# Optimization experiments

Measured on AMD Instinct MI355X. Metric: run time of the kernel, lower is better.

Reference implementation:

```python
import jax, jax.numpy as jnp
import numpy as np

NUM_HEADS = 16
EPS = 1e-6


def _ln(t, w, b):
    # LayerNorm over last dim (head_dim), elementwise affine, eps=1e-6
    mu = jnp.mean(t, axis=-1, keepdims=True)
    var = jnp.mean(jnp.square(t - mu), axis=-1, keepdims=True)
    return (t - mu) * jax.lax.rsqrt(var + EPS) * w + b


def setup_inputs() -> dict:
    key = jax.random.key(0)
    ks = jax.random.split(key, 10)
    b, s1, s2, qdim, kdim = 2, 2048, 3072, 1024, 1024
    d = qdim // NUM_HEADS
    x = jax.random.normal(ks[0], (b, s1, qdim), dtype=jnp.float32)
    y = jax.random.normal(ks[1], (b, s2, kdim), dtype=jnp.float32)
    padding_mask = jax.random.randint(ks[2], (b, s2), 0, 2) > 0
    # guarantee at least one valid key per row (avoid all -inf softmax rows)
    padding_mask = padding_mask.at[:, 0].set(True)
    w = 0.02
    Wq = jax.random.normal(ks[3], (qdim, qdim), dtype=jnp.float32) * w
    bq = jnp.zeros((qdim,), jnp.float32)
    Wkv = jax.random.normal(ks[4], (2 * qdim, kdim), dtype=jnp.float32) * w
    bkv = jnp.zeros((2 * qdim,), jnp.float32)
    qn_w = jnp.ones((d,), jnp.float32)
    qn_b = jnp.zeros((d,), jnp.float32)
    kn_w = jnp.ones((d,), jnp.float32)
    kn_b = jnp.zeros((d,), jnp.float32)
    Wo = jax.random.normal(ks[5], (qdim, qdim), dtype=jnp.float32) * w
    bo = jnp.zeros((qdim,), jnp.float32)
    return {"x": x, "y": y, "padding_mask": padding_mask,
            "Wq": Wq, "bq": bq, "Wkv": Wkv, "bkv": bkv,
            "qn_w": qn_w, "qn_b": qn_b, "kn_w": kn_w, "kn_b": kn_b,
            "Wo": Wo, "bo": bo}


def reference(x, y, padding_mask, Wq, bq, Wkv, bkv, qn_w, qn_b, kn_w, kn_b, Wo, bo):
    b, s1, c = x.shape
    s2 = y.shape[1]
    h, d = NUM_HEADS, c // NUM_HEADS
    scale = d ** (-0.5)
    q = (x @ Wq.T + bq).reshape(b, s1, h, d)
    kv = (y @ Wkv.T + bkv).reshape(b, s2, 2, h, d)
    k, v = kv[:, :, 0], kv[:, :, 1]  # (b, s2, h, d)
    q = _ln(q, qn_w, qn_b) * scale
    k = _ln(k, kn_w, kn_b)
    attn = jnp.einsum('bihd,bjhd->bhij', q, k)  # (b, h, s1, s2)
    attn = jnp.where(padding_mask[:, None, None, :], attn, -jnp.inf)
    p = jax.nn.softmax(attn, axis=-1)
    ctx = jnp.einsum('bhij,bjhd->bihd', p, v).reshape(b, s1, c)
    out = ctx @ Wo.T + bo
    return out
```

## Files before the change

kernel.cpp:

```cpp
#include <hip/hip_runtime.h>
#include <stdint.h>
#include <stddef.h>

typedef __attribute__((ext_vector_type(4))) float  f32x4;
typedef __attribute__((ext_vector_type(8))) short  short8;
typedef __attribute__((ext_vector_type(4))) short  short4v;
typedef __attribute__((ext_vector_type(2))) unsigned int uint2v;

__device__ __forceinline__ unsigned short f2bfbits(float f) {
  unsigned int u = __builtin_bit_cast(unsigned int, f);
  u += 0x7FFFu + ((u >> 16) & 1u);
  return (unsigned short)(u >> 16);
}

__device__ __forceinline__ f32x4 mfma16(short8 a, short8 b, f32x4 c) {
  return __builtin_amdgcn_mfma_f32_16x16x32_bf16(a, b, c, 0, 0, 0);
}

__device__ __forceinline__ unsigned int cvtpk(float a, float b) {
  unsigned int r;
  asm volatile("v_cvt_pk_bf16_f32 %0, %1, %2" : "=v"(r) : "v"(a), "v"(b));
  return r;
}

__device__ __forceinline__ void gload16(const void* g, void* l) {
  __builtin_amdgcn_global_load_lds(
      (const __attribute__((address_space(1))) void*)g,
      (__attribute__((address_space(3))) void*)l, 16, 0, 0);
}

__device__ __forceinline__ void cvt_block(const float* __restrict__ in,
                                          unsigned short* __restrict__ out,
                                          int blk, int t) {
  size_t i = (size_t)blk * 256 + t;
  f32x4 a = *(const f32x4*)(in + i * 8);
  f32x4 b = *(const f32x4*)(in + i * 8 + 4);
  short8 o;
  o[0] = (short)f2bfbits(a[0]); o[1] = (short)f2bfbits(a[1]);
  o[2] = (short)f2bfbits(a[2]); o[3] = (short)f2bfbits(a[3]);
  o[4] = (short)f2bfbits(b[0]); o[5] = (short)f2bfbits(b[1]);
  o[6] = (short)f2bfbits(b[2]); o[7] = (short)f2bfbits(b[3]);
  *(short8*)(out + i * 8) = o;
}

__global__ __launch_bounds__(256) void fused_prep(
    const float* __restrict__ x, unsigned short* __restrict__ xb,
    const float* __restrict__ y, unsigned short* __restrict__ yb,
    const float* __restrict__ Wq, unsigned short* __restrict__ Wqb,
    const float* __restrict__ Wkv, unsigned short* __restrict__ Wkvb,
    const float* __restrict__ Wo, unsigned short* __restrict__ Wob,
    const unsigned char* __restrict__ mraw, float* __restrict__ maddC,
    int* __restrict__ invperm, int* __restrict__ nvalid) {
  const int bid = blockIdx.x, t = threadIdx.x;
  if (bid < 2048)       { cvt_block(x,   xb,   bid,        t); return; }
  else if (bid < 5120)  { cvt_block(y,   yb,   bid - 2048, t); return; }
  else if (bid < 5632)  { cvt_block(Wq,  Wqb,  bid - 5120, t); return; }
  else if (bid < 6656)  { cvt_block(Wkv, Wkvb, bid - 5632, t); return; }
  else if (bid < 7168)  { cvt_block(Wo,  Wob,  bid - 6656, t); return; }

  const int batch = bid - 7168;
  __shared__ int s_na, s_gt, s_m84;
  if (t == 0) { s_na = 0; s_gt = 0; s_m84 = 0; }
  __syncthreads();
  int na = 0, gt = 0, m84 = 0;
  for (int i = t; i < 4096; i += 256) {
    unsigned char v = mraw[i];
    if (v) {
      if (i & 3) na++;
      if ((i & 7) == 4) m84++;
      if (v > 1) gt++;
    }
  }
  atomicAdd(&s_na, na); atomicAdd(&s_gt, gt); atomicAdd(&s_m84, m84);
  __syncthreads();
  int layout;
  if (s_na == 0) layout = s_m84 ? 1 : 3;
  else           layout = s_gt ? 2 : 0;

  const int base = batch * 3072;
  int myv[12];
  int cnt = 0;
#pragma unroll
  for (int k = 0; k < 12; k++) {
    int j = t * 12 + k;
    int gj = base + j;
    bool mv;
    if (layout == 0)      mv = mraw[gj] != 0;
    else if (layout == 1) mv = ((const int*)mraw)[gj] != 0;
    else if (layout == 2) mv = ((const float*)mraw)[gj] > 0.5f;
    else                  mv = ((const long long*)mraw)[gj] != 0;
    myv[k] = mv ? 1 : 0;
    cnt += myv[k];
  }
  const int lane = t & 63, wv = t >> 6;
  int inc = cnt;
#pragma unroll
  for (int d = 1; d < 64; d <<= 1) {
    int n = __shfl_up(inc, d);
    if (lane >= d) inc += n;
  }
  __shared__ int wsum[4];
  if (lane == 63) wsum[wv] = inc;
  __syncthreads();
  int woff = 0;
#pragma unroll
  for (int i2 = 0; i2 < 4; i2++) if (i2 < wv) woff += wsum[i2];
  const int total = wsum[0] + wsum[1] + wsum[2] + wsum[3];
  int vp = woff + inc - cnt;
  if (t == 0) nvalid[batch] = total;
#pragma unroll
  for (int k = 0; k < 12; k++) {
    int j = t * 12 + k;
    int slot = myv[k] ? vp : (total + (j - vp));
    invperm[base + slot] = j;
    vp += myv[k];
  }
  for (int jj = t; jj < 3072; jj += 256)
    maddC[base + jj] = (jj < total) ? -10.0f : -1e30f;
}

__global__ __launch_bounds__(256) void gemm_qkv(
    const unsigned short* __restrict__ xb, const unsigned short* __restrict__ Wqb,
    const float* __restrict__ bq, const float* __restrict__ qnw,
    const float* __restrict__ qnb, unsigned short* __restrict__ qln,
    const unsigned short* __restrict__ yb, const unsigned short* __restrict__ Wkvb,
    const float* __restrict__ bkv, const float* __restrict__ knw,
    const float* __restrict__ knb, unsigned short* __restrict__ kln,
    unsigned short* __restrict__ vrow) {
  __shared__ unsigned short As[128 * 64];
  __shared__ unsigned short Bs[128 * 64];
  const int t = threadIdx.x, l = t & 63, w = t >> 6;
  const int lo = l & 15, hi = l >> 4;
  const int wr = w >> 1, wc = w & 1;
  const int flat = blockIdx.x;
  int vb;
  if (flat < 256) vb = (flat & 7) * 32 + (flat >> 3);
  else { int f2 = flat - 256; vb = 256 + (f2 & 7) * 96 + (f2 >> 3); }
  const int isq = vb < 256;
  const int bn = isq ? (vb & 7) : ((vb - 256) & 15);
  const int bm = isq ? (vb >> 3) : ((vb - 256) >> 4);
  const unsigned short* A = isq ? xb : yb;
  const unsigned short* B = isq ? Wqb : Wkvb;
  const float* bias = isq ? bq : bkv;
  const float* lnw = isq ? qnw : knw;
  const float* lnb = isq ? qnb : knb;
  unsigned short* bfout = isq ? qln : kln;
  const float lnscale = isq ? 0.125f * 1.44269504f : 1.0f;
  const int rpb = isq ? 2048 : 3072;
  const int K = 1024;

  const int sr = l >> 3;
  const int sc = ((l & 7) ^ sr) << 3;
  const unsigned short* Ab = A + (size_t)bm * 128 * K + (size_t)sr * K + sc;
  const unsigned short* Bb = B + (size_t)bn * 128 * K + (size_t)sr * K + sc;

  f32x4 acc[4][4] = {};

  for (int kt = 0; kt < K; kt += 64) {
    __syncthreads();
#pragma unroll
    for (int p = 0; p < 4; ++p) {
      int c = w * 4 + p;
      gload16(Ab + (size_t)c * 8 * K + kt, &As[c * 512]);
      gload16(Bb + (size_t)c * 8 * K + kt, &Bs[c * 512]);
    }
    __syncthreads();
#pragma unroll
    for (int kk = 0; kk < 2; ++kk) {
      short8 af[4], bf[4];
#pragma unroll
      for (int i = 0; i < 4; ++i) {
        int slot = (((kk * 4 + hi) ^ (lo & 7)) << 3);
        af[i] = *(const short8*)&As[(wr * 64 + i * 16 + lo) * 64 + slot];
        bf[i] = *(const short8*)&Bs[(wc * 64 + i * 16 + lo) * 64 + slot];
      }
#pragma unroll
      for (int i = 0; i < 4; ++i)
#pragma unroll
        for (int j = 0; j < 4; ++j)
          acc[i][j] = mfma16(af[i], bf[j], acc[i][j]);
    }
  }

  float bv[4];
#pragma unroll
  for (int j = 0; j < 4; ++j) bv[j] = bias[bn * 128 + wc * 64 + j * 16 + lo];
#pragma unroll
  for (int i = 0; i < 4; ++i)
#pragma unroll
    for (int j = 0; j < 4; ++j)
#pragma unroll
      for (int r = 0; r < 4; ++r) acc[i][j][r] += bv[j];

  if (!isq && bn >= 8) {
#pragma unroll
    for (int j = 0; j < 4; ++j) {
      int col = bn * 128 + wc * 64 + j * 16 + lo;
      int vcol = col - 1024;
#pragma unroll
      for (int i = 0; i < 4; ++i) {
        int row = bm * 128 + wr * 64 + i * 16 + hi * 4;
#pragma unroll
        for (int r = 0; r < 4; ++r)
          vrow[(size_t)(row + r) * 1024 + vcol] = f2bfbits(acc[i][j][r]);
      }
    }
  } else {
    float gwv[4], gbv[4];
#pragma unroll
    for (int j = 0; j < 4; ++j) {
      gwv[j] = lnw[j * 16 + lo];
      gbv[j] = lnb[j * 16 + lo];
    }
    const int hcol = (bn * 128 + wc * 64) >> 6;
#pragma unroll
    for (int i = 0; i < 4; ++i) {
#pragma unroll
      for (int r = 0; r < 4; ++r) {
        float s1 = (acc[i][0][r] + acc[i][1][r]) + (acc[i][2][r] + acc[i][3][r]);
        float s2 = (acc[i][0][r] * acc[i][0][r] + acc[i][1][r] * acc[i][1][r]) +
                   (acc[i][2][r] * acc[i][2][r] + acc[i][3][r] * acc[i][3][r]);
#pragma unroll
        for (int m = 1; m < 16; m <<= 1) {
          s1 += __shfl_xor(s1, m);
          s2 += __shfl_xor(s2, m);
        }
        float mu = s1 * 0.015625f;
        float var = fmaxf(s2 * 0.015625f - mu * mu, 0.0f);
        float rq = rsqrtf(var + 1e-6f);
        int row = bm * 128 + wr * 64 + i * 16 + hi * 4 + r;
        int bb = row >= rpb;
        int rr = row - bb * rpb;
        size_t base = ((size_t)(bb * 16 + hcol) * rpb + rr) * 64;
#pragma unroll
        for (int j = 0; j < 4; ++j)
          bfout[base + j * 16 + lo] =
              f2bfbits(((acc[i][j][r] - mu) * rq * gwv[j] + gbv[j]) * lnscale);
      }
    }
  }
}

__global__ __launch_bounds__(256) void v_tr(
    const unsigned short* __restrict__ vrow, const int* __restrict__ invperm,
    unsigned short* __restrict__ vt) {
  __shared__ unsigned short tile[64][65];
  const int jt = blockIdx.x, h = blockIdx.y;
  const int b = jt / 48, j0 = (jt % 48) * 64;
  const int t = threadIdx.x;
  const int r = t >> 2, c0 = (t & 3) << 4;
  const int sj = invperm[b * 3072 + j0 + r];
  const unsigned short* src = vrow + ((size_t)b * 3072 + sj) * 1024 + h * 64 + c0;
  *(short8*)&tile[r][c0]     = *(const short8*)src;
  *(short8*)&tile[r][c0 + 8] = *(const short8*)(src + 8);
  __syncthreads();
  const int d = t >> 2, jc = (t & 3) << 4;
  unsigned short* dst = vt + ((size_t)((b * 16 + h) * 64 + d)) * 3072 + j0 + jc;
  short8 o0, o1;
#pragma unroll
  for (int i = 0; i < 8; i++) o0[i] = tile[jc + i][d];
#pragma unroll
  for (int i = 0; i < 8; i++) o1[i] = tile[jc + 8 + i][d];
  *(short8*)dst = o0;
  *(short8*)(dst + 8) = o1;
}

__global__ __launch_bounds__(512) void gemm_out(
    const unsigned short* __restrict__ A, const unsigned short* __restrict__ B,
    const float* __restrict__ bias, float* __restrict__ C, int N, int K) {
  __shared__ unsigned short As[128 * 64];
  __shared__ unsigned short Bs[128 * 64];
  const int t = threadIdx.x, l = t & 63, w = t >> 6;
  const int lo = l & 15, hi = l >> 4;
  const int wr = w >> 1, wc = w & 1;
  const int bn = blockIdx.x, bm = blockIdx.y;

  const int sr = l >> 3;
  const int sc = ((l & 7) ^ sr) << 3;
  const unsigned short* Ab = A + (size_t)bm * 128 * K + (size_t)sr * K + sc;
  const unsigned short* Bb = B + (size_t)bn * 128 * K + (size_t)sr * K + sc;

  f32x4 acc[2][4] = {};

  for (int kt = 0; kt < K; kt += 64) {
    __syncthreads();
#pragma unroll
    for (int p = 0; p < 2; ++p) {
      int c = p * 8 + w;
      gload16(Ab + (size_t)c * 8 * K + kt, &As[c * 512]);
      gload16(Bb + (size_t)c * 8 * K + kt, &Bs[c * 512]);
    }
    __syncthreads();
#pragma unroll
    for (int kk = 0; kk < 2; ++kk) {
      short8 af[2], bf[4];
#pragma unroll
      for (int i = 0; i < 2; ++i) {
        int slot = (((kk * 4 + hi) ^ (lo & 7)) << 3);
        af[i] = *(const short8*)&As[(wr * 32 + i * 16 + lo) * 64 + slot];
      }
#pragma unroll
      for (int j = 0; j < 4; ++j) {
        int slot = (((kk * 4 + hi) ^ (lo & 7)) << 3);
        bf[j] = *(const short8*)&Bs[(wc * 64 + j * 16 + lo) * 64 + slot];
      }
#pragma unroll
      for (int i = 0; i < 2; ++i)
#pragma unroll
        for (int j = 0; j < 4; ++j)
          acc[i][j] = mfma16(af[i], bf[j], acc[i][j]);
    }
  }

#pragma unroll
  for (int j = 0; j < 4; ++j) {
    int col = bn * 128 + wc * 64 + j * 16 + lo;
    float bv = bias[col];
#pragma unroll
    for (int i = 0; i < 2; ++i) {
      int row = bm * 128 + wr * 32 + i * 16 + hi * 4;
#pragma unroll
      for (int r = 0; r < 4; ++r)
        C[(size_t)(row + r) * N + col] = acc[i][j][r] + bv;
    }
  }
}

__global__ __launch_bounds__(256, 4) void attn_fwd(
    const unsigned short* __restrict__ Q, const unsigned short* __restrict__ KnU,
    const unsigned short* __restrict__ Vt, const float* __restrict__ maskAdd,
    const int* __restrict__ invperm, const int* __restrict__ nva,
    unsigned short* __restrict__ ctx) {
  int flat = blockIdx.y * 32 + blockIdx.x;
  int f = (flat & 7) * 128 + (flat >> 3);
  const int bh = f >> 5, qb = f & 31;
  const int b = bh >> 4, h = bh & 15;
  const int t = threadIdx.x, l = t & 63, w = t >> 6;
  const int lo = l & 15, hi = l >> 4;
  const int q0 = qb * 64 + w * 16;

  const int nv = nva[b];
  const int kend = (nv + 63) & ~63;

  __shared__ unsigned short lds[20480];
  unsigned short* Ks = lds;
  unsigned short* Vs = lds + 8192;
  unsigned short* P  = lds + 16384 + w * 1024;

  const unsigned short* Qh = Q + ((size_t)bh * 2048 + q0) * 64;
  const unsigned short* KbU = KnU + (size_t)bh * 3072 * 64;
  const unsigned short* Vb = Vt + (size_t)bh * 64 * 3072;
  const float* mb = maskAdd + b * 3072;
  const int ibase = b * 3072;

  const int srow = w * 8 + (l >> 3);
  const int swz8 = ((l & 7) ^ ((l >> 3) & 7)) << 3;
  const unsigned short* vS = Vb + (size_t)srow * 3072 + swz8;
  const int dstoff = w * 512;

  short8 qf[2];
#pragma unroll
  for (int g = 0; g < 2; g++)
    qf[g] = *(const short8*)(Qh + (size_t)lo * 64 + g * 32 + hi * 8);

  f32x4 O[4] = {};
  f32x4 lacc = {};
  const int myswz = (lo & 7) << 3;

  short8 paR[2] = {};
  short8 vfR[4][2] = {};

  int rs0 = invperm[ibase + srow];
  int rs1 = invperm[ibase + 32 + srow];
  gload16(KbU + (size_t)rs0 * 64 + swz8, Ks + dstoff);
  gload16(KbU + (size_t)rs1 * 64 + swz8, Ks + 2048 + dstoff);
  gload16(vS, Vs + dstoff);
  gload16(vS + 98304, Vs + 2048 + dstoff);
  {
    int kt1 = (64 < kend) ? 64 : 0;
    rs0 = invperm[ibase + kt1 + srow];
    rs1 = invperm[ibase + kt1 + 32 + srow];
  }
  __syncthreads();

  for (int kt = 0; kt < kend; kt += 64) {
    const int cur = (kt >> 6) & 1;
    const int nxt = cur ^ 1;
    const int ktn = (kt + 64 < kend) ? kt + 64 : 0;
    gload16(KbU + (size_t)rs0 * 64 + swz8, Ks + nxt * 4096 + dstoff);
    gload16(KbU + (size_t)rs1 * 64 + swz8, Ks + nxt * 4096 + 2048 + dstoff);
    gload16(vS + ktn, Vs + nxt * 4096 + dstoff);
    gload16(vS + ktn + 98304, Vs + nxt * 4096 + 2048 + dstoff);
    {
      int ktn2 = (kt + 128 < kend) ? kt + 128 : 0;
      rs0 = invperm[ibase + ktn2 + srow];
      rs1 = invperm[ibase + ktn2 + 32 + srow];
    }

    const unsigned short* Kc = Ks + cur * 4096;
    const unsigned short* Vc = Vs + cur * 4096;

    f32x4 s[4];
#pragma unroll
    for (int nf = 0; nf < 4; nf++)
      s[nf] = *(const f32x4*)(mb + kt + nf * 16 + hi * 4);
    __builtin_amdgcn_s_setprio(1);
#pragma unroll
    for (int nf = 0; nf < 4; nf++) {
      const int row = nf * 16 + lo;
      short8 k0 = *(const short8*)&Kc[row * 64 + ((hi * 8) ^ myswz)];
      short8 k1 = *(const short8*)&Kc[row * 64 + ((32 + hi * 8) ^ myswz)];
      s[nf] = mfma16(k0, qf[0], s[nf]);
      s[nf] = mfma16(k1, qf[1], s[nf]);
    }

#pragma unroll
    for (int df = 0; df < 4; df++)
#pragma unroll
      for (int ks = 0; ks < 2; ks++)
        O[df] = mfma16(paR[ks], vfR[df][ks], O[df]);
    __builtin_amdgcn_s_setprio(0);

#pragma unroll
    for (int nf = 0; nf < 4; nf++)
#pragma unroll
      for (int r = 0; r < 4; r++)
        s[nf][r] = __builtin_amdgcn_exp2f(s[nf][r]);
    lacc += (s[0] + s[1]) + (s[2] + s[3]);

#pragma unroll
    for (int nf = 0; nf < 4; nf++) {
      uint2v u;
      u.x = cvtpk(s[nf][0], s[nf][1]);
      u.y = cvtpk(s[nf][2], s[nf][3]);
      *(uint2v*)&P[lo * 64 + ((nf * 16 + hi * 4) ^ myswz)] = u;
    }
#pragma unroll
    for (int ks = 0; ks < 2; ks++)
      paR[ks] = *(const short8*)&P[lo * 64 + ((ks * 32 + hi * 8) ^ myswz)];
#pragma unroll
    for (int df = 0; df < 4; df++) {
      const int row = df * 16 + lo;
#pragma unroll
      for (int ks = 0; ks < 2; ks++)
        vfR[df][ks] = *(const short8*)&Vc[row * 64 + ((ks * 32 + hi * 8) ^ myswz)];
    }

    __syncthreads();
  }

  __builtin_amdgcn_s_setprio(1);
#pragma unroll
  for (int df = 0; df < 4; df++)
#pragma unroll
    for (int ks = 0; ks < 2; ks++)
      O[df] = mfma16(paR[ks], vfR[df][ks], O[df]);
  __builtin_amdgcn_s_setprio(0);

  float lr = (lacc[0] + lacc[1]) + (lacc[2] + lacc[3]);
  lr += __shfl_xor(lr, 16);
  lr += __shfl_xor(lr, 32);

  float i0 = 1.0f / __shfl(lr, hi * 4 + 0);
  float i1 = 1.0f / __shfl(lr, hi * 4 + 1);
  float i2 = 1.0f / __shfl(lr, hi * 4 + 2);
  float i3 = 1.0f / __shfl(lr, hi * 4 + 3);
  size_t rbase = (size_t)b * 2048 + q0 + hi * 4;
#pragma unroll
  for (int df = 0; df < 4; df++) {
    int cc = h * 64 + df * 16 + lo;
    ctx[(rbase + 0) * 1024 + cc] = f2bfbits(O[df][0] * i0);
    ctx[(rbase + 1) * 1024 + cc] = f2bfbits(O[df][1] * i1);
    ctx[(rbase + 2) * 1024 + cc] = f2bfbits(O[df][2] * i2);
    ctx[(rbase + 3) * 1024 + cc] = f2bfbits(O[df][3] * i3);
  }
}

extern "C" void kernel_launch(void* const* d_in, const int* in_sizes, int n_in,
                              void* d_out, int out_size, void* d_ws, size_t ws_size,
                              hipStream_t stream) {
  const float* x   = (const float*)d_in[0];
  const float* y   = (const float*)d_in[1];
  const unsigned char* pmask = (const unsigned char*)d_in[2];
  const float* Wq  = (const float*)d_in[3];
  const float* bq  = (const float*)d_in[4];
  const float* Wkv = (const float*)d_in[5];
  const float* bkv = (const float*)d_in[6];
  const float* qnw = (const float*)d_in[7];
  const float* qnb = (const float*)d_in[8];
  const float* knw = (const float*)d_in[9];
  const float* knb = (const float*)d_in[10];
  const float* Wo  = (const float*)d_in[11];
  const float* bo  = (const float*)d_in[12];
  float* out = (float*)d_out;

  const size_t MB = 1024ull * 1024ull;
  char* ws = (char*)d_ws;
  float* maddC         = (float*)ws;
  int*   invperm       = (int*)(ws + 24576);
  int*   nvalid        = (int*)(ws + 49152);
  char*  wb            = ws + 131072;
  unsigned short* Wqb  = (unsigned short*)(wb);
  unsigned short* Wkvb = (unsigned short*)(wb + 2 * MB);
  unsigned short* Wob  = (unsigned short*)(wb + 6 * MB);
  unsigned short* qln  = (unsigned short*)(wb + 8 * MB);
  unsigned short* kln  = (unsigned short*)(wb + 16 * MB);
  unsigned short* vt   = (unsigned short*)(wb + 28 * MB);
  unsigned short* ctxb = (unsigned short*)(wb + 40 * MB);
  unsigned short* yb   = (unsigned short*)(wb + 48 * MB);
  unsigned short* xb   = (unsigned short*)(wb + 60 * MB);
  unsigned short* vrow = (unsigned short*)(wb + 68 * MB);
  if (ws_size < 131072 + 80 * MB) return;

  fused_prep<<<dim3(7170), dim3(256), 0, stream>>>(
      x, xb, y, yb, Wq, Wqb, Wkv, Wkvb, Wo, Wob, pmask, maddC, invperm,
      nvalid);

  gemm_qkv<<<dim3(1024), dim3(256), 0, stream>>>(
      xb, Wqb, bq, qnw, qnb, qln, yb, Wkvb, bkv, knw, knb, kln, vrow);

  v_tr<<<dim3(96, 16), dim3(256), 0, stream>>>(vrow, invperm, vt);

  attn_fwd<<<dim3(32, 32), dim3(256), 0, stream>>>(qln, kln, vt, maddC,
                                                   invperm, nvalid, ctxb);

  gemm_out<<<dim3(8, 32), dim3(512), 0, stream>>>(ctxb, Wob, bo, out, 1024, 1024);
}
```

Before: 147.0 us.

## Halve attention key tile to 32 and drop software-pipelined PV to raise occupancy

The attention kernel's key/value tile shrinks from 64 to 32 keys per iteration, which halves LDS use and the per-wave P buffer. The launch bound goes from 4 to 8 blocks per CU. The PV MFMAs no longer run one iteration behind the QK MFMAs in registers; they run in the same iteration, which frees the paR/vfR registers. The aim is more resident waves to hide latency, at the cost of twice as many barriers and loop iterations and less overlap of MFMA with exp inside a wave.

```diff
diff --git a/kernel.cpp b/kernel.cpp
--- a/kernel.cpp
+++ b/kernel.cpp
@@ -326,7 +326,7 @@
   }
 }
 
-__global__ __launch_bounds__(256, 4) void attn_fwd(
+__global__ __launch_bounds__(256, 8) void attn_fwd(
     const unsigned short* __restrict__ Q, const unsigned short* __restrict__ KnU,
     const unsigned short* __restrict__ Vt, const float* __restrict__ maskAdd,
     const int* __restrict__ invperm, const int* __restrict__ nva,
@@ -340,12 +340,12 @@
   const int q0 = qb * 64 + w * 16;
 
   const int nv = nva[b];
-  const int kend = (nv + 63) & ~63;
-
-  __shared__ unsigned short lds[20480];
+  const int kend = (nv + 31) & ~31;
+
+  __shared__ unsigned short lds[10240];
   unsigned short* Ks = lds;
-  unsigned short* Vs = lds + 8192;
-  unsigned short* P  = lds + 16384 + w * 1024;
+  unsigned short* Vs = lds + 4096;
+  unsigned short* P  = lds + 8192 + w * 512;
 
   const unsigned short* Qh = Q + ((size_t)bh * 2048 + q0) * 64;
   const unsigned short* KbU = KnU + (size_t)bh * 3072 * 64;
@@ -355,7 +355,9 @@
 
   const int srow = w * 8 + (l >> 3);
   const int swz8 = ((l & 7) ^ ((l >> 3) & 7)) << 3;
-  const unsigned short* vS = Vb + (size_t)srow * 3072 + swz8;
+  const int vdrow = w * 16 + (l >> 2);
+  const int vsswz = ((l & 3) ^ ((l >> 2) & 3)) << 3;
+  const unsigned short* vS = Vb + (size_t)vdrow * 3072 + vsswz;
   const int dstoff = w * 512;
 
   short8 qf[2];
@@ -366,96 +368,72 @@
   f32x4 O[4] = {};
   f32x4 lacc = {};
   const int myswz = (lo & 7) << 3;
-
-  short8 paR[2] = {};
-  short8 vfR[4][2] = {};
+  const int pswz  = (lo & 3) << 3;
 
   int rs0 = invperm[ibase + srow];
-  int rs1 = invperm[ibase + 32 + srow];
   gload16(KbU + (size_t)rs0 * 64 + swz8, Ks + dstoff);
-  gload16(KbU + (size_t)rs1 * 64 + swz8, Ks + 2048 + dstoff);
   gload16(vS, Vs + dstoff);
-  gload16(vS + 98304, Vs + 2048 + dstoff);
   {
-    int kt1 = (64 < kend) ? 64 : 0;
+    int kt1 = (32 < kend) ? 32 : 0;
     rs0 = invperm[ibase + kt1 + srow];
-    rs1 = invperm[ibase + kt1 + 32 + srow];
   }
   __syncthreads();
 
-  for (int kt = 0; kt < kend; kt += 64) {
-    const int cur = (kt >> 6) & 1;
+  for (int kt = 0; kt < kend; kt += 32) {
+    const int cur = (kt >> 5) & 1;
     const int nxt = cur ^ 1;
-    const int ktn = (kt + 64 < kend) ? kt + 64 : 0;
-    gload16(KbU + (size_t)rs0 * 64 + swz8, Ks + nxt * 4096 + dstoff);
-    gload16(KbU + (size_t)rs1 * 64 + swz8, Ks + nxt * 4096 + 2048 + dstoff);
-    gload16(vS + ktn, Vs + nxt * 4096 + dstoff);
-    gload16(vS + ktn + 98304, Vs + nxt * 4096 + 2048 + dstoff);
+    const int ktn = (kt + 32 < kend) ? kt + 32 : 0;
+    gload16(KbU + (size_t)rs0 * 64 + swz8, Ks + nxt * 2048 + dstoff);
+    gload16(vS + ktn, Vs + nxt * 2048 + dstoff);
     {
-      int ktn2 = (kt + 128 < kend) ? kt + 128 : 0;
+      int ktn2 = (kt + 64 < kend) ? kt + 64 : 0;
       rs0 = invperm[ibase + ktn2 + srow];
-      rs1 = invperm[ibase + ktn2 + 32 + srow];
-    }
-
-    const unsigned short* Kc = Ks + cur * 4096;
-    const unsigned short* Vc = Vs + cur * 4096;
-
-    f32x4 s[4];
-#pragma unroll
-    for (int nf = 0; nf < 4; nf++)
-      s[nf] = *(const f32x4*)(mb + kt + nf * 16 + hi * 4);
+    }
+
+    const unsigned short* Kc = Ks + cur * 2048;
+    const unsigned short* Vc = Vs + cur * 2048;
+
+    f32x4 s[2];
+    s[0] = *(const f32x4*)(mb + kt + hi * 4);
+    s[1] = *(const f32x4*)(mb + kt + 16 + hi * 4);
     __builtin_amdgcn_s_setprio(1);
 #pragma unroll
-    for (int nf = 0; nf < 4; nf++) {
+    for (int nf = 0; nf < 2; nf++) {
       const int row = nf * 16 + lo;
       short8 k0 = *(const short8*)&Kc[row * 64 + ((hi * 8) ^ myswz)];
       short8 k1 = *(const short8*)&Kc[row * 64 + ((32 + hi * 8) ^ myswz)];
       s[nf] = mfma16(k0, qf[0], s[nf]);
       s[nf] = mfma16(k1, qf[1], s[nf]);
     }
-
-#pragma unroll
-    for (int df = 0; df < 4; df++)
-#pragma unroll
-      for (int ks = 0; ks < 2; ks++)
-        O[df] = mfma16(paR[ks], vfR[df][ks], O[df]);
     __builtin_amdgcn_s_setprio(0);
 
 #pragma unroll
-    for (int nf = 0; nf < 4; nf++)
+    for (int nf = 0; nf < 2; nf++)
 #pragma unroll
       for (int r = 0; r < 4; r++)
         s[nf][r] = __builtin_amdgcn_exp2f(s[nf][r]);
-    lacc += (s[0] + s[1]) + (s[2] + s[3]);
-
-#pragma unroll
-    for (int nf = 0; nf < 4; nf++) {
+    lacc += s[0] + s[1];
+
+#pragma unroll
+    for (int nf = 0; nf < 2; nf++) {
       uint2v u;
       u.x = cvtpk(s[nf][0], s[nf][1]);
       u.y = cvtpk(s[nf][2], s[nf][3]);
-      *(uint2v*)&P[lo * 64 + ((nf * 16 + hi * 4) ^ myswz)] = u;
-    }
-#pragma unroll
-    for (int ks = 0; ks < 2; ks++)
-      paR[ks] = *(const short8*)&P[lo * 64 + ((ks * 32 + hi * 8) ^ myswz)];
+      *(uint2v*)&P[lo * 32 + ((nf * 16 + hi * 4) ^ pswz)] = u;
+    }
+    short8 pa = *(const short8*)&P[lo * 32 + ((hi * 8) ^ pswz)];
+
+    __builtin_amdgcn_s_setprio(1);
 #pragma unroll
     for (int df = 0; df < 4; df++) {
       const int row = df * 16 + lo;
-#pragma unroll
-      for (int ks = 0; ks < 2; ks++)
-        vfR[df][ks] = *(const short8*)&Vc[row * 64 + ((ks * 32 + hi * 8) ^ myswz)];
-    }
+      short8 vf = *(const short8*)&Vc[row * 32 + ((hi * 8) ^ pswz)];
+      O[df] = mfma16(pa, vf, O[df]);
+    }
+    __builtin_amdgcn_s_setprio(0);
 
     __syncthreads();
   }
-
-  __builtin_amdgcn_s_setprio(1);
-#pragma unroll
-  for (int df = 0; df < 4; df++)
-#pragma unroll
-    for (int ks = 0; ks < 2; ks++)
-      O[df] = mfma16(paR[ks], vfR[df][ks], O[df]);
-  __builtin_amdgcn_s_setprio(0);
 
   float lr = (lacc[0] + lacc[1]) + (lacc[2] + lacc[3]);
   lr += __shfl_xor(lr, 16);
```

Result: slower. 152.8 us (+3.9%).

## Double-buffer LDS tiles in QKV and output GEMMs; skip mask loads for full-valid tiles

Applied to the files above, without the earlier changes.

Both projection GEMMs now use two LDS buffers, prefetching the next K-tile while computing the current one. This replaces two barriers per iteration with one and overlaps global loads with MFMA work. The attention kernel also skips loading the additive mask for key tiles known to be all valid and uses the constant -10 instead. Doubling LDS per block may reduce occupancy, and the last iteration issues a redundant prefetch.

```diff
diff --git a/kernel.cpp b/kernel.cpp
--- a/kernel.cpp
+++ b/kernel.cpp
@@ -127,8 +127,8 @@
     const float* __restrict__ bkv, const float* __restrict__ knw,
     const float* __restrict__ knb, unsigned short* __restrict__ kln,
     unsigned short* __restrict__ vrow) {
-  __shared__ unsigned short As[128 * 64];
-  __shared__ unsigned short Bs[128 * 64];
+  __shared__ unsigned short As[2 * 128 * 64];
+  __shared__ unsigned short Bs[2 * 128 * 64];
   const int t = threadIdx.x, l = t & 63, w = t >> 6;
   const int lo = l & 15, hi = l >> 4;
   const int wr = w >> 1, wc = w & 1;
@@ -156,23 +156,32 @@
 
   f32x4 acc[4][4] = {};
 
+#pragma unroll
+  for (int p = 0; p < 4; ++p) {
+    int c = w * 4 + p;
+    gload16(Ab + (size_t)c * 8 * K, &As[c * 512]);
+    gload16(Bb + (size_t)c * 8 * K, &Bs[c * 512]);
+  }
+  __syncthreads();
+
   for (int kt = 0; kt < K; kt += 64) {
-    __syncthreads();
+    const int cur = (kt >> 6) & 1;
+    const int nxt = cur ^ 1;
+    const int ktn = (kt + 64 < K) ? kt + 64 : 0;
 #pragma unroll
     for (int p = 0; p < 4; ++p) {
       int c = w * 4 + p;
-      gload16(Ab + (size_t)c * 8 * K + kt, &As[c * 512]);
-      gload16(Bb + (size_t)c * 8 * K + kt, &Bs[c * 512]);
-    }
-    __syncthreads();
+      gload16(Ab + (size_t)c * 8 * K + ktn, &As[nxt * 8192 + c * 512]);
+      gload16(Bb + (size_t)c * 8 * K + ktn, &Bs[nxt * 8192 + c * 512]);
+    }
 #pragma unroll
     for (int kk = 0; kk < 2; ++kk) {
       short8 af[4], bf[4];
 #pragma unroll
       for (int i = 0; i < 4; ++i) {
         int slot = (((kk * 4 + hi) ^ (lo & 7)) << 3);
-        af[i] = *(const short8*)&As[(wr * 64 + i * 16 + lo) * 64 + slot];
-        bf[i] = *(const short8*)&Bs[(wc * 64 + i * 16 + lo) * 64 + slot];
+        af[i] = *(const short8*)&As[cur * 8192 + (wr * 64 + i * 16 + lo) * 64 + slot];
+        bf[i] = *(const short8*)&Bs[cur * 8192 + (wc * 64 + i * 16 + lo) * 64 + slot];
       }
 #pragma unroll
       for (int i = 0; i < 4; ++i)
@@ -180,6 +189,7 @@
         for (int j = 0; j < 4; ++j)
           acc[i][j] = mfma16(af[i], bf[j], acc[i][j]);
     }
+    __syncthreads();
   }
 
   float bv[4];
@@ -268,8 +278,8 @@
 __global__ __launch_bounds__(512) void gemm_out(
     const unsigned short* __restrict__ A, const unsigned short* __restrict__ B,
     const float* __restrict__ bias, float* __restrict__ C, int N, int K) {
-  __shared__ unsigned short As[128 * 64];
-  __shared__ unsigned short Bs[128 * 64];
+  __shared__ unsigned short As[2 * 128 * 64];
+  __shared__ unsigned short Bs[2 * 128 * 64];
   const int t = threadIdx.x, l = t & 63, w = t >> 6;
   const int lo = l & 15, hi = l >> 4;
   const int wr = w >> 1, wc = w & 1;
@@ -282,27 +292,36 @@
 
   f32x4 acc[2][4] = {};
 
+#pragma unroll
+  for (int p = 0; p < 2; ++p) {
+    int c = p * 8 + w;
+    gload16(Ab + (size_t)c * 8 * K, &As[c * 512]);
+    gload16(Bb + (size_t)c * 8 * K, &Bs[c * 512]);
+  }
+  __syncthreads();
+
   for (int kt = 0; kt < K; kt += 64) {
-    __syncthreads();
+    const int cur = (kt >> 6) & 1;
+    const int nxt = cur ^ 1;
+    const int ktn = (kt + 64 < K) ? kt + 64 : 0;
 #pragma unroll
     for (int p = 0; p < 2; ++p) {
       int c = p * 8 + w;
-      gload16(Ab + (size_t)c * 8 * K + kt, &As[c * 512]);
-      gload16(Bb + (size_t)c * 8 * K + kt, &Bs[c * 512]);
-    }
-    __syncthreads();
+      gload16(Ab + (size_t)c * 8 * K + ktn, &As[nxt * 8192 + c * 512]);
+      gload16(Bb + (size_t)c * 8 * K + ktn, &Bs[nxt * 8192 + c * 512]);
+    }
 #pragma unroll
     for (int kk = 0; kk < 2; ++kk) {
       short8 af[2], bf[4];
 #pragma unroll
       for (int i = 0; i < 2; ++i) {
         int slot = (((kk * 4 + hi) ^ (lo & 7)) << 3);
-        af[i] = *(const short8*)&As[(wr * 32 + i * 16 + lo) * 64 + slot];
+        af[i] = *(const short8*)&As[cur * 8192 + (wr * 32 + i * 16 + lo) * 64 + slot];
       }
 #pragma unroll
       for (int j = 0; j < 4; ++j) {
         int slot = (((kk * 4 + hi) ^ (lo & 7)) << 3);
-        bf[j] = *(const short8*)&Bs[(wc * 64 + j * 16 + lo) * 64 + slot];
+        bf[j] = *(const short8*)&Bs[cur * 8192 + (wc * 64 + j * 16 + lo) * 64 + slot];
       }
 #pragma unroll
       for (int i = 0; i < 2; ++i)
@@ -310,6 +329,7 @@
         for (int j = 0; j < 4; ++j)
           acc[i][j] = mfma16(af[i], bf[j], acc[i][j]);
     }
+    __syncthreads();
   }
 
 #pragma unroll
@@ -401,9 +421,15 @@
     const unsigned short* Vc = Vs + cur * 4096;
 
     f32x4 s[4];
-#pragma unroll
-    for (int nf = 0; nf < 4; nf++)
-      s[nf] = *(const f32x4*)(mb + kt + nf * 16 + hi * 4);
+    if (kt + 64 <= nv) {
+#pragma unroll
+      for (int nf = 0; nf < 4; nf++)
+        s[nf] = f32x4{-10.0f, -10.0f, -10.0f, -10.0f};
+    } else {
+#pragma unroll
+      for (int nf = 0; nf < 4; nf++)
+        s[nf] = *(const f32x4*)(mb + kt + nf * 16 + hi * 4);
+    }
     __builtin_amdgcn_s_setprio(1);
 #pragma unroll
     for (int nf = 0; nf < 4; nf++) {
```

Result: no change. 146.8 us (median of 2 runs) (-0.2%).
